# Performance work log

Measured on AMD Instinct MI355X. Metric: run time of the kernel, lower is better.

Reference implementation:

```python
import jax, jax.numpy as jnp
import numpy as np

EPS = 1e-5  # torch BatchNorm1d default eps
NUM_CLASSES = 10


def setup_inputs() -> dict:
    key = jax.random.key(0)
    ks = jax.random.split(key, 8)
    N, M, D = 8192, 8192, 256
    h1, h2 = 128, 64
    x = jax.random.normal(ks[0], (N, D), dtype=jnp.float32)
    x_n = jax.random.normal(ks[1], (M, D), dtype=jnp.float32)
    y_n = jax.random.randint(ks[2], (M,), 0, NUM_CLASSES)
    # Linear weights (torch layout [out, in]) and biases
    W0 = jax.random.normal(ks[3], (h1, D), dtype=jnp.float32) * 0.05
    b0 = jnp.zeros((h1,), dtype=jnp.float32)
    W1 = jax.random.normal(ks[4], (h2, h1), dtype=jnp.float32) * 0.05
    b1 = jnp.zeros((h2,), dtype=jnp.float32)
    # BatchNorm1d affine params (torch init: weight=1, bias=0)
    g0 = jnp.ones((h1,), dtype=jnp.float32)
    bt0 = jnp.zeros((h1,), dtype=jnp.float32)
    g1 = jnp.ones((h2,), dtype=jnp.float32)
    bt1 = jnp.zeros((h2,), dtype=jnp.float32)
    return {"x": x, "x_n": x_n, "y_n": y_n,
            "W0": W0, "b0": b0, "g0": g0, "bt0": bt0,
            "W1": W1, "b1": b1, "g1": g1, "bt1": bt1}


def _bn(h, gamma, beta):
    # BatchNorm1d in training mode: batch mean / biased batch var per feature
    m = jnp.mean(h, axis=0)
    v = jnp.var(h, axis=0)
    return gamma * (h - m) / jnp.sqrt(v + EPS) + beta


def _feats(z, params):
    # fcn stack: BatchNorm(Tanh(Linear(z)))
    for W, b, g, bt in params:
        z = _bn(jnp.tanh(z @ W.T + b), g, bt)
    return z


def reference(x, x_n, y_n, W0, b0, g0, bt0, W1, b1, g1, bt1):
    params = [(W0, b0, g0, bt0), (W1, b1, g1, bt1)]
    q = _feats(x, params)    # [N, 64]
    k = _feats(x_n, params)  # [M, 64]
    # euclidean cdist via the quadratic expansion
    d2 = (jnp.sum(q * q, axis=1)[:, None]
          + jnp.sum(k * k, axis=1)[None, :]
          - 2.0 * (q @ k.T))
    sim = jnp.sqrt(jnp.maximum(d2, 1e-12))  # [N, M]
    sim = jnp.max(sim) - sim                 # larger = nearer
    # x != x_n here, so no self-mask branch (matches torch.equal check)
    p = jax.nn.softmax(sim, axis=1)          # [N, M]
    y1h = jax.nn.one_hot(y_n, NUM_CLASSES, dtype=p.dtype)  # [M, C]
    return jnp.clip(p @ y1h, 0.0, 1.0)       # [N, C]
```

## Files before the change

### kernel.cpp

```cpp
#include <hip/hip_runtime.h>
#include <math.h>

#define EPSBN 1e-5f
#define AADD(p, v) __hip_atomic_fetch_add((p), (v), __ATOMIC_RELAXED, __HIP_MEMORY_SCOPE_AGENT)

typedef unsigned short u16;
typedef short bf16x8 __attribute__((ext_vector_type(8)));
typedef float f32x4 __attribute__((ext_vector_type(4)));
typedef float f32x16 __attribute__((ext_vector_type(16)));

constexpr int NROWS = 8192;
constexpr int NCLS = 10;
constexpr int MPAD = 8832;
constexpr int NT_PAD = 138;
constexpr int GY = 8;
constexpr float SCL  = 2.0813689810056077f;
constexpr float SCL2 = -4.1627379620112154f;

constexpr size_t OFF_W0P = 0;
constexpr size_t OFF_H1H = 32768;
constexpr size_t OFF_H1L = OFF_H1H + 1048576;
constexpr size_t OFF_SUM = OFF_H1L + 1048576;
constexpr size_t OFF_W1P = OFF_SUM + 768;
constexpr size_t OFF_B1E = OFF_W1P + 16384;
constexpr size_t OFF_H2  = OFF_B1E + 128;
constexpr size_t OFF_PIDX = OFF_H2 + 1048576;
constexpr size_t OFF_TCLS = OFF_PIDX + MPAD;
constexpr size_t OFF_QB  = OFF_H1H;
constexpr size_t OFF_KB  = OFF_QB + 262144;
constexpr size_t OFF_QN2 = OFF_KB + 282624;
constexpr size_t OFF_KN2 = OFF_QN2 + NROWS;
constexpr size_t OFF_PART = OFF_H2;

__device__ inline u16 f2bf(float f) {
  unsigned u = __float_as_uint(f);
  unsigned r = (u + 0x7fffu + ((u >> 16) & 1u)) >> 16;
  return (u16)r;
}
__device__ inline float bf2f(u16 h) { return __uint_as_float(((unsigned)h) << 16); }

__device__ inline float tanh_fast(float x) {
  float e = __builtin_amdgcn_exp2f(x * 2.88539008f);
  return 1.f - 2.f * __builtin_amdgcn_rcpf(e + 1.f);
}

__device__ inline void glds16(const u16* g, u16* l) {
  __builtin_amdgcn_global_load_lds(
      (const __attribute__((address_space(1))) unsigned int*)g,
      (__attribute__((address_space(3))) unsigned int*)l, 16, 0, 0);
}

__global__ __launch_bounds__(256) void k_prep(
    const float* __restrict__ w0, const int* __restrict__ yn,
    u16* __restrict__ w0p, int* __restrict__ pidx, int* __restrict__ tcls,
    float* __restrict__ sums)
{
  const int B = blockIdx.x;
  const int tid = threadIdx.x;
  if (B < 128) {
    int idx = B * 256 + tid;
    int t = idx & 255;
    float v = w0[idx];
    u16 hi = f2bf(v);
    u16 lo = f2bf(v - bf2f(hi));
    int j = idx >> 8;
    w0p[(t >> 3) * 1024 + j * 8 + (t & 7)] = hi;
    w0p[32768 + (t >> 3) * 1024 + j * 8 + (t & 7)] = lo;
    return;
  }

  __shared__ int cnt[256][NCLS];
  __shared__ int counts[NCLS];
  __shared__ int pst[NCLS + 1];
  const int lane = tid & 63, wv = tid >> 6;
  #pragma unroll
  for (int c = 0; c < NCLS; ++c) cnt[tid][c] = 0;
  __syncthreads();
  for (int i = tid; i < NROWS; i += 256) cnt[tid][yn[i]]++;
  __syncthreads();
  if (tid < NCLS) {
    int s = 0;
    for (int t = 0; t < 256; ++t) s += cnt[t][tid];
    counts[tid] = s;
  }
  __syncthreads();
  if (tid == 0) {
    int run = 0;
    #pragma unroll
    for (int c = 0; c < NCLS; ++c) {
      pst[c] = run;
      run += ((counts[c] + 63) >> 6) << 6;
    }
    pst[NCLS] = run;
  }
  __syncthreads();

  if (B == 128) {
    sums[tid] = 0.f; sums[tid + 256] = 0.f; sums[tid + 512] = 0.f;
    if (tid == 0) {
      #pragma unroll
      for (int c = 0; c < NCLS; ++c) {
        int nt = (counts[c] + 63) >> 6;
        for (int tt = 0; tt < nt; ++tt) tcls[(pst[c] >> 6) + tt] = c;
      }
      for (int tt = pst[NCLS] >> 6; tt < NT_PAD; ++tt) tcls[tt] = NCLS;
    }
    for (int i = tid; i < MPAD; i += 256) {
      bool pad;
      if (i >= pst[NCLS]) pad = true;
      else {
        int c = 0;
        while (i >= pst[c + 1]) ++c;
        pad = (i >= pst[c] + counts[c]);
      }
      if (pad) pidx[i] = -1;
    }
    return;
  }

  const int c = B - 129;
  __shared__ int wsum[4];
  int x = cnt[tid][c];
  int inc = x;
  #pragma unroll
  for (int d = 1; d < 64; d <<= 1) { int y = __shfl_up(inc, d); if (lane >= d) inc += y; }
  if (lane == 63) wsum[wv] = inc;
  __syncthreads();
  int add = 0;
  for (int w2 = 0; w2 < 4; ++w2) if (w2 < wv) add += wsum[w2];
  int base = pst[c] + (inc - x) + add;
  for (int i = tid; i < NROWS; i += 256) {
    if (yn[i] == c) pidx[base++] = i;
  }
}

__global__ __launch_bounds__(256) void k_layer1(
    const float* __restrict__ x, const float* __restrict__ xn,
    const u16* __restrict__ w0p, const float* __restrict__ b0,
    u16* __restrict__ h1h, u16* __restrict__ h1l, float* __restrict__ sums)
{
  const int tid = threadIdx.x;
  const int w = tid >> 6, l = tid & 63;
  const int l15 = l & 15, l4 = l >> 4;
  const int blk = blockIdx.x;
  const int rowHalf = w & 1, colHalf = w >> 1;
  const int r0 = blk * 32 + 16 * rowHalf;
  const int c0 = 64 * colHalf;
  const int b = (blk < 256) ? 0 : 1;
  const float* src = (blk < 256) ? (x + (size_t)blk * 32 * 256)
                                 : (xn + (size_t)(blk - 256) * 32 * 256);
  const float* xrow = src + (size_t)(16 * rowHalf + l15) * 256;

  f32x4 acc[4];
  #pragma unroll
  for (int ct = 0; ct < 4; ++ct) acc[ct] = (f32x4){0.f, 0.f, 0.f, 0.f};

  #pragma unroll
  for (int ks = 0; ks < 8; ++ks) {
    const float* xp = xrow + ks * 32 + l4 * 8;
    f32x4 a0 = *(const f32x4*)xp;
    f32x4 a1 = *(const f32x4*)(xp + 4);
    bf16x8 ah, al_;
    #pragma unroll
    for (int i = 0; i < 4; ++i) {
      u16 h = f2bf(a0[i]); ah[i] = (short)h; al_[i] = (short)f2bf(a0[i] - bf2f(h));
    }
    #pragma unroll
    for (int i = 0; i < 4; ++i) {
      u16 h = f2bf(a1[i]); ah[4 + i] = (short)h; al_[4 + i] = (short)f2bf(a1[i] - bf2f(h));
    }
    const u16* bbase = w0p + (size_t)(ks * 4 + l4) * 1024;
    #pragma unroll
    for (int ct = 0; ct < 4; ++ct) {
      const int col = c0 + 16 * ct + l15;
      bf16x8 bh = *(const bf16x8*)(bbase + col * 8);
      bf16x8 bl = *(const bf16x8*)(bbase + 32768 + col * 8);
      acc[ct] = __builtin_amdgcn_mfma_f32_16x16x32_bf16(ah, bh, acc[ct], 0, 0, 0);
      acc[ct] = __builtin_amdgcn_mfma_f32_16x16x32_bf16(ah, bl, acc[ct], 0, 0, 0);
      acc[ct] = __builtin_amdgcn_mfma_f32_16x16x32_bf16(al_, bh, acc[ct], 0, 0, 0);
    }
  }

  #pragma unroll
  for (int ct = 0; ct < 4; ++ct) {
    const int col = c0 + 16 * ct + l15;
    const float bj = b0[col];
    float s = 0.f, q = 0.f;
    #pragma unroll
    for (int r = 0; r < 4; ++r) {
      float v = tanh_fast(acc[ct][r] + bj);
      const int row = r0 + 4 * l4 + r;
      u16 hi = f2bf(v);
      h1h[(size_t)row * 128 + col] = hi;
      h1l[(size_t)row * 128 + col] = f2bf(v - bf2f(hi));
      s += v; q += v * v;
    }
    s += __shfl_xor(s, 16); s += __shfl_xor(s, 32);
    q += __shfl_xor(q, 16); q += __shfl_xor(q, 32);
    if (l < 16) {
      AADD(&sums[b * 128 + col], s);
      AADD(&sums[256 + b * 128 + col], q);
    }
  }
}

__global__ __launch_bounds__(128) void k_foldp(
    const float* __restrict__ w1, const float* __restrict__ b1,
    const float* __restrict__ g0, const float* __restrict__ bt0,
    const float* __restrict__ sums, u16* __restrict__ w1p, float* __restrict__ b1e)
{
  const int o = blockIdx.x;
  const int j = threadIdx.x;
  __shared__ float red[2][2];
  const float w = w1[o * 128 + j];
  #pragma unroll
  for (int b = 0; b < 2; ++b) {
    float s = sums[b * 128 + j], q = sums[256 + b * 128 + j];
    float m = s * (1.f / 8192.f);
    float v = q * (1.f / 8192.f) - m * m;
    float sc = g0[j] * rsqrtf(v + EPSBN);
    float sh = bt0[j] - m * sc;
    float wsc = w * sc;
    u16 hi = f2bf(wsc);
    u16 lo = f2bf(wsc - bf2f(hi));
    w1p[((size_t)(b * 2 + 0) * 16 + (j >> 3)) * 512 + o * 8 + (j & 7)] = hi;
    w1p[((size_t)(b * 2 + 1) * 16 + (j >> 3)) * 512 + o * 8 + (j & 7)] = lo;
    float a = w * sh;
    #pragma unroll
    for (int off = 32; off; off >>= 1) a += __shfl_xor(a, off);
    if ((j & 63) == 0) red[j >> 6][b] = a;
  }
  __syncthreads();
  if (j < 2) b1e[j * 64 + o] = b1[o] + red[0][j] + red[1][j];
}

__global__ __launch_bounds__(256) void k_layer2(
    const u16* __restrict__ h1h, const u16* __restrict__ h1l,
    const u16* __restrict__ w1p, const float* __restrict__ b1e,
    float* __restrict__ h2, float* __restrict__ sums)
{
  const int tid = threadIdx.x;
  const int w = tid >> 6, l = tid & 63;
  const int l15 = l & 15, l4 = l >> 4;
  const int blk = blockIdx.x;
  const int rowHalf = w & 1, colHalf = w >> 1;
  const int r0 = blk * 32 + 16 * rowHalf;
  const int c0 = 32 * colHalf;
  const int b = blk >> 8;
  const u16* arow_h = h1h + (size_t)(r0 + l15) * 128;
  const u16* arow_l = h1l + (size_t)(r0 + l15) * 128;

  f32x4 acc[2];
  acc[0] = (f32x4){0.f, 0.f, 0.f, 0.f};
  acc[1] = (f32x4){0.f, 0.f, 0.f, 0.f};

  #pragma unroll
  for (int ks = 0; ks < 4; ++ks) {
    bf16x8 ah = *(const bf16x8*)(arow_h + ks * 32 + l4 * 8);
    bf16x8 al_ = *(const bf16x8*)(arow_l + ks * 32 + l4 * 8);
    const u16* bb = w1p + ((size_t)(b * 2) * 16 + ks * 4 + l4) * 512;
    #pragma unroll
    for (int ct = 0; ct < 2; ++ct) {
      const int col = c0 + 16 * ct + l15;
      bf16x8 bh = *(const bf16x8*)(bb + col * 8);
      bf16x8 bl = *(const bf16x8*)(bb + 8192 + col * 8);
      acc[ct] = __builtin_amdgcn_mfma_f32_16x16x32_bf16(ah, bh, acc[ct], 0, 0, 0);
      acc[ct] = __builtin_amdgcn_mfma_f32_16x16x32_bf16(ah, bl, acc[ct], 0, 0, 0);
      acc[ct] = __builtin_amdgcn_mfma_f32_16x16x32_bf16(al_, bh, acc[ct], 0, 0, 0);
    }
  }

  #pragma unroll
  for (int ct = 0; ct < 2; ++ct) {
    const int col = c0 + 16 * ct + l15;
    const float bj = b1e[b * 64 + col];
    float s = 0.f, q = 0.f;
    #pragma unroll
    for (int r = 0; r < 4; ++r) {
      float v = tanh_fast(acc[ct][r] + bj);
      const int row = r0 + 4 * l4 + r;
      h2[(size_t)row * 64 + col] = v;
      s += v; q += v * v;
    }
    s += __shfl_xor(s, 16); s += __shfl_xor(s, 32);
    q += __shfl_xor(q, 16); q += __shfl_xor(q, 32);
    if (l < 16) {
      AADD(&sums[512 + b * 64 + col], s);
      AADD(&sums[640 + b * 64 + col], q);
    }
  }
}

__global__ __launch_bounds__(256) void k_bn2(
    const float* __restrict__ h2, const float* __restrict__ sums,
    const float* __restrict__ g1, const float* __restrict__ bt1,
    const int* __restrict__ pidx,
    u16* __restrict__ qb, float* __restrict__ qn2,
    u16* __restrict__ kb, float* __restrict__ kn2)
{
  const int tid = threadIdx.x;
  const int r = tid >> 6, o = tid & 63;
  const bool isq = (blockIdx.x < 2048);
  const int b = isq ? 0 : 1;
  float s = sums[512 + b * 64 + o], q = sums[640 + b * 64 + o];
  float m = s * (1.f / 8192.f);
  float v = q * (1.f / 8192.f) - m * m;
  float sc = g1[o] * rsqrtf(v + EPSBN);
  float sh = bt1[o] - m * sc;
  if (isq) {
    const int row = blockIdx.x * 4 + r;
    float vv = sc * h2[(size_t)row * 64 + o] + sh;
    qb[(size_t)row * 64 + o] = f2bf(vv);
    float sq = vv * vv;
    #pragma unroll
    for (int off = 32; off; off >>= 1) sq += __shfl_xor(sq, off);
    if (o == 0) qn2[row] = SCL * sq;
  } else {
    const int row = (blockIdx.x - 2048) * 4 + r;
    const int src = pidx[row];
    float vv = 0.f;
    if (src >= 0) vv = sc * h2[(size_t)(NROWS + src) * 64 + o] + sh;
    kb[(size_t)row * 64 + o] = f2bf(vv);
    float sq = vv * vv;
    #pragma unroll
    for (int off = 32; off; off >>= 1) sq += __shfl_xor(sq, off);
    if (o == 0) kn2[row] = (src >= 0) ? SCL * sq : 1e30f;
  }
}

__global__ __launch_bounds__(256, 4) void k_dist(
    const u16* __restrict__ qb, const float* __restrict__ qn2,
    const u16* __restrict__ kb, const float* __restrict__ kn2,
    const int* __restrict__ tcls, float* __restrict__ part)
{
  __shared__ u16 bs[3][4096];
  __shared__ float cls_lds[2 * (NCLS + 1) * 64];
  const int tid = threadIdx.x;
  const int w = tid >> 6, l = tid & 63;
  const int n0 = blockIdx.x * 64;
  const int g = blockIdx.y;
  const int t0 = (g * NT_PAD) / GY, t1 = ((g + 1) * NT_PAD) / GY;

  for (int i = tid; i < 2 * (NCLS + 1) * 64; i += 256) cls_lds[i] = 0.f;

  const int lh = l >> 5;
  const int rb = w >> 1, ch = w & 1;
  const int arow = n0 + 32 * rb + (l & 31);
  bf16x8 aB[4];
  #pragma unroll
  for (int j = 0; j < 4; ++j)
    aB[j] = *(const bf16x8*)(qb + (size_t)arow * 64 + j * 16 + 8 * lh);
  float qnr[16];
  #pragma unroll
  for (int g4 = 0; g4 < 4; ++g4) {
    f32x4 qv = *(const f32x4*)(qn2 + n0 + 32 * rb + 8 * g4 + 4 * lh);
    qnr[4*g4+0] = qv[0]; qnr[4*g4+1] = qv[1]; qnr[4*g4+2] = qv[2]; qnr[4*g4+3] = qv[3];
  }

  int soff[2];
  #pragma unroll
  for (int q = 0; q < 2; ++q)
    soff[q] = (16 * w + 8 * q + (l >> 3)) * 64 + ((l & 7) ^ (l >> 3)) * 8;

  const int colL = 32 * ch + (l & 31);
  const int c7 = colL & 7;

#define STAGE(TT, PB) do { const u16* gp_ = kb + (size_t)(TT) * 4096; \
    u16* lb_ = &bs[PB][0] + w * 1024; \
    glds16(gp_ + soff[0], lb_); \
    glds16(gp_ + soff[1], lb_ + 512); } while (0)

#define FLUSH(CC) do { \
    _Pragma("unroll") for (int r = 0; r < 16; ++r) { \
      run[r] += __shfl_xor(run[r], 1);  run[r] += __shfl_xor(run[r], 2); \
      run[r] += __shfl_xor(run[r], 4);  run[r] += __shfl_xor(run[r], 8); \
      run[r] += __shfl_xor(run[r], 16); } \
    if ((l & 31) == 0) { \
      float* cl_ = cls_lds + ch * 704 + (CC) * 64 + 32 * rb + 4 * lh; \
      _Pragma("unroll") for (int r = 0; r < 16; ++r) cl_[(r & 3) + 8 * (r >> 2)] += run[r]; } \
    _Pragma("unroll") for (int r = 0; r < 16; ++r) run[r] = 0.f; } while (0)

  STAGE(t0, 0);
  if (t0 + 1 < t1) STAGE(t0 + 1, 1);

  float run[16];
  #pragma unroll
  for (int r = 0; r < 16; ++r) run[r] = 0.f;
  int ccur = tcls[t0];
  int p = 0;

  for (int t = t0; t < t1; ++t) {
    if (t + 1 < t1) { asm volatile("s_waitcnt vmcnt(2)" ::: "memory"); }
    else            { asm volatile("s_waitcnt vmcnt(0)" ::: "memory"); }
    __builtin_amdgcn_s_barrier();
    asm volatile("" ::: "memory");

    if (t + 2 < t1) { int pb2 = p + 2; if (pb2 >= 3) pb2 -= 3; STAGE(t + 2, pb2); }

    const int c = tcls[t];
    if (c != ccur) { FLUSH(ccur); ccur = c; }
    const float kv = kn2[t * 64 + colL];

    f32x16 acc0, acc1;
    #pragma unroll
    for (int r = 0; r < 16; ++r) { acc0[r] = 0.f; acc1[r] = 0.f; }
    const char* pb_ = (const char*)&bs[p][0] + colL * 128;
    {
      bf16x8 b0_ = *(const bf16x8*)(pb_ + (((0 + lh) ^ c7) << 4));
      bf16x8 b1_ = *(const bf16x8*)(pb_ + (((2 + lh) ^ c7) << 4));
      bf16x8 b2_ = *(const bf16x8*)(pb_ + (((4 + lh) ^ c7) << 4));
      bf16x8 b3_ = *(const bf16x8*)(pb_ + (((6 + lh) ^ c7) << 4));
      acc0 = __builtin_amdgcn_mfma_f32_32x32x16_bf16(aB[0], b0_, acc0, 0, 0, 0);
      acc1 = __builtin_amdgcn_mfma_f32_32x32x16_bf16(aB[1], b1_, acc1, 0, 0, 0);
      acc0 = __builtin_amdgcn_mfma_f32_32x32x16_bf16(aB[2], b2_, acc0, 0, 0, 0);
      acc1 = __builtin_amdgcn_mfma_f32_32x32x16_bf16(aB[3], b3_, acc1, 0, 0, 0);
    }
    #pragma unroll
    for (int r = 0; r < 16; ++r) {
      float d2 = fmaf(SCL2, acc0[r] + acc1[r], qnr[r] + kv);
      d2 = fmaxf(d2, 2.0813689e-12f);
      run[r] += __builtin_amdgcn_exp2f(-__builtin_amdgcn_sqrtf(d2));
    }
    p = (p == 2) ? 0 : p + 1;
  }
  FLUSH(ccur);
  __syncthreads();

  for (int i = tid; i < (NCLS + 1) * 64; i += 256) {
    const int c = i >> 6, rr = i & 63;
    part[((size_t)g * (NCLS + 1) + c) * NROWS + n0 + rr] = cls_lds[i] + cls_lds[704 + i];
  }
#undef STAGE
#undef FLUSH
}

__global__ __launch_bounds__(256) void k_final(const float* __restrict__ part,
                                               float* __restrict__ out)
{
  const int n = blockIdx.x * 256 + threadIdx.x;
  float sc[NCLS];
  #pragma unroll
  for (int c = 0; c < NCLS; ++c) sc[c] = 0.f;
  for (int g = 0; g < GY; ++g) {
    #pragma unroll
    for (int c = 0; c < NCLS; ++c)
      sc[c] += part[((size_t)g * (NCLS + 1) + c) * NROWS + n];
  }
  float tot = 0.f;
  #pragma unroll
  for (int c = 0; c < NCLS; ++c) tot += sc[c];
  const float inv = 1.f / tot;
  #pragma unroll
  for (int c = 0; c < NCLS; ++c)
    out[(size_t)n * NCLS + c] = fminf(fmaxf(sc[c] * inv, 0.f), 1.f);
}

extern "C" void kernel_launch(void* const* d_in, const int* in_sizes, int n_in,
                              void* d_out, int out_size, void* d_ws, size_t ws_size,
                              hipStream_t stream) {
  const float* x   = (const float*)d_in[0];
  const float* xn  = (const float*)d_in[1];
  const int*   yn  = (const int*)d_in[2];
  const float* W0  = (const float*)d_in[3];
  const float* b0  = (const float*)d_in[4];
  const float* g0  = (const float*)d_in[5];
  const float* bt0 = (const float*)d_in[6];
  const float* W1  = (const float*)d_in[7];
  const float* b1  = (const float*)d_in[8];
  const float* g1  = (const float*)d_in[9];
  const float* bt1 = (const float*)d_in[10];
  float* out = (float*)d_out;
  float* ws  = (float*)d_ws;

  u16*   w0pp = (u16*)(ws + OFF_W0P);
  u16*   h1hp = (u16*)(ws + OFF_H1H);
  u16*   h1lp = (u16*)(ws + OFF_H1L);
  float* sumsp= ws + OFF_SUM;
  u16*   w1pp = (u16*)(ws + OFF_W1P);
  float* b1ep = ws + OFF_B1E;
  float* h2p  = ws + OFF_H2;
  int*   pidxp= (int*)(ws + OFF_PIDX);
  int*   tclsp= (int*)(ws + OFF_TCLS);
  u16*   qbp  = (u16*)(ws + OFF_QB);
  float* qn2p = ws + OFF_QN2;
  u16*   kbp  = (u16*)(ws + OFF_KB);
  float* kn2p = ws + OFF_KN2;
  float* partp= ws + OFF_PART;

  k_prep<<<139, 256, 0, stream>>>(W0, yn, w0pp, pidxp, tclsp, sumsp);
  k_layer1<<<512, 256, 0, stream>>>(x, xn, w0pp, b0, h1hp, h1lp, sumsp);
  k_foldp<<<64, 128, 0, stream>>>(W1, b1, g0, bt0, sumsp, w1pp, b1ep);
  k_layer2<<<512, 256, 0, stream>>>(h1hp, h1lp, w1pp, b1ep, h2p, sumsp);
  k_bn2<<<2048 + MPAD / 4, 256, 0, stream>>>(h2p, sumsp, g1, bt1, pidxp,
                                             qbp, qn2p, kbp, kn2p);
  k_dist<<<dim3(128, GY), 256, 0, stream>>>(qbp, qn2p, kbp, kn2p, tclsp, partp);
  k_final<<<32, 256, 0, stream>>>(partp, out);
}
```

Baseline: 140.9 us.

## Fuse BN1 weight folding into layer2 kernel and double dist grid Y

Removes the separate k_foldp launch. Each layer2 block now computes the BN1 scale and shift from the sums, builds the split bf16 hi/lo folded W1 in shared memory, and computes the folded bias itself. This saves one launch and a global round trip, but repeats the fold work in all 512 blocks and adds a serial 128-step bias loop in 64 threads. Separately, GY for the distance kernel grid goes from 8 to 16, and the partial buffer moves to its own workspace region so it no longer aliases h2.

```diff
diff --git a/kernel.cpp b/kernel.cpp
--- a/kernel.cpp
+++ b/kernel.cpp
@@ -13,7 +13,7 @@
 constexpr int NCLS = 10;
 constexpr int MPAD = 8832;
 constexpr int NT_PAD = 138;
-constexpr int GY = 8;
+constexpr int GY = 16;
 constexpr float SCL  = 2.0813689810056077f;
 constexpr float SCL2 = -4.1627379620112154f;
 
@@ -21,16 +21,14 @@
 constexpr size_t OFF_H1H = 32768;
 constexpr size_t OFF_H1L = OFF_H1H + 1048576;
 constexpr size_t OFF_SUM = OFF_H1L + 1048576;
-constexpr size_t OFF_W1P = OFF_SUM + 768;
-constexpr size_t OFF_B1E = OFF_W1P + 16384;
-constexpr size_t OFF_H2  = OFF_B1E + 128;
+constexpr size_t OFF_H2  = OFF_SUM + 768;
 constexpr size_t OFF_PIDX = OFF_H2 + 1048576;
 constexpr size_t OFF_TCLS = OFF_PIDX + MPAD;
+constexpr size_t OFF_PART = OFF_TCLS + 144;
 constexpr size_t OFF_QB  = OFF_H1H;
 constexpr size_t OFF_KB  = OFF_QB + 262144;
 constexpr size_t OFF_QN2 = OFF_KB + 282624;
 constexpr size_t OFF_KN2 = OFF_QN2 + NROWS;
-constexpr size_t OFF_PART = OFF_H2;
 
 __device__ inline u16 f2bf(float f) {
   unsigned u = __float_as_uint(f);
@@ -204,41 +202,14 @@
   }
 }
 
-__global__ __launch_bounds__(128) void k_foldp(
-    const float* __restrict__ w1, const float* __restrict__ b1,
-    const float* __restrict__ g0, const float* __restrict__ bt0,
-    const float* __restrict__ sums, u16* __restrict__ w1p, float* __restrict__ b1e)
-{
-  const int o = blockIdx.x;
-  const int j = threadIdx.x;
-  __shared__ float red[2][2];
-  const float w = w1[o * 128 + j];
-  #pragma unroll
-  for (int b = 0; b < 2; ++b) {
-    float s = sums[b * 128 + j], q = sums[256 + b * 128 + j];
-    float m = s * (1.f / 8192.f);
-    float v = q * (1.f / 8192.f) - m * m;
-    float sc = g0[j] * rsqrtf(v + EPSBN);
-    float sh = bt0[j] - m * sc;
-    float wsc = w * sc;
-    u16 hi = f2bf(wsc);
-    u16 lo = f2bf(wsc - bf2f(hi));
-    w1p[((size_t)(b * 2 + 0) * 16 + (j >> 3)) * 512 + o * 8 + (j & 7)] = hi;
-    w1p[((size_t)(b * 2 + 1) * 16 + (j >> 3)) * 512 + o * 8 + (j & 7)] = lo;
-    float a = w * sh;
-    #pragma unroll
-    for (int off = 32; off; off >>= 1) a += __shfl_xor(a, off);
-    if ((j & 63) == 0) red[j >> 6][b] = a;
-  }
-  __syncthreads();
-  if (j < 2) b1e[j * 64 + o] = b1[o] + red[0][j] + red[1][j];
-}
-
 __global__ __launch_bounds__(256) void k_layer2(
     const u16* __restrict__ h1h, const u16* __restrict__ h1l,
-    const u16* __restrict__ w1p, const float* __restrict__ b1e,
+    const float* __restrict__ W1, const float* __restrict__ b1,
+    const float* __restrict__ g0, const float* __restrict__ bt0,
     float* __restrict__ h2, float* __restrict__ sums)
 {
+  __shared__ u16 w1l[16384];
+  __shared__ float sc0s[128], sh0s[128], b1es[64];
   const int tid = threadIdx.x;
   const int w = tid >> 6, l = tid & 63;
   const int l15 = l & 15, l4 = l >> 4;
@@ -247,6 +218,31 @@
   const int r0 = blk * 32 + 16 * rowHalf;
   const int c0 = 32 * colHalf;
   const int b = blk >> 8;
+
+  if (tid < 128) {
+    float s = sums[b * 128 + tid], q = sums[256 + b * 128 + tid];
+    float m = s * (1.f / 8192.f);
+    float v = q * (1.f / 8192.f) - m * m;
+    float sc = g0[tid] * rsqrtf(v + EPSBN);
+    sc0s[tid] = sc;
+    sh0s[tid] = bt0[tid] - m * sc;
+  }
+  __syncthreads();
+  for (int e = tid; e < 8192; e += 256) {
+    const int j = e >> 6, o = e & 63;
+    float wv = W1[o * 128 + j];
+    float wsc = wv * sc0s[j];
+    u16 hi = f2bf(wsc);
+    w1l[(j >> 3) * 512 + o * 8 + (j & 7)] = hi;
+    w1l[8192 + (j >> 3) * 512 + o * 8 + (j & 7)] = f2bf(wsc - bf2f(hi));
+  }
+  if (tid < 64) {
+    float a = 0.f;
+    for (int j = 0; j < 128; ++j) a = fmaf(W1[tid * 128 + j], sh0s[j], a);
+    b1es[tid] = b1[tid] + a;
+  }
+  __syncthreads();
+
   const u16* arow_h = h1h + (size_t)(r0 + l15) * 128;
   const u16* arow_l = h1l + (size_t)(r0 + l15) * 128;
 
@@ -258,7 +254,7 @@
   for (int ks = 0; ks < 4; ++ks) {
     bf16x8 ah = *(const bf16x8*)(arow_h + ks * 32 + l4 * 8);
     bf16x8 al_ = *(const bf16x8*)(arow_l + ks * 32 + l4 * 8);
-    const u16* bb = w1p + ((size_t)(b * 2) * 16 + ks * 4 + l4) * 512;
+    const u16* bb = w1l + (size_t)(ks * 4 + l4) * 512;
     #pragma unroll
     for (int ct = 0; ct < 2; ++ct) {
       const int col = c0 + 16 * ct + l15;
@@ -273,7 +269,7 @@
   #pragma unroll
   for (int ct = 0; ct < 2; ++ct) {
     const int col = c0 + 16 * ct + l15;
-    const float bj = b1e[b * 64 + col];
+    const float bj = b1es[col];
     float s = 0.f, q = 0.f;
     #pragma unroll
     for (int r = 0; r < 4; ++r) {
@@ -476,21 +472,18 @@
   u16*   h1hp = (u16*)(ws + OFF_H1H);
   u16*   h1lp = (u16*)(ws + OFF_H1L);
   float* sumsp= ws + OFF_SUM;
-  u16*   w1pp = (u16*)(ws + OFF_W1P);
-  float* b1ep = ws + OFF_B1E;
   float* h2p  = ws + OFF_H2;
   int*   pidxp= (int*)(ws + OFF_PIDX);
   int*   tclsp= (int*)(ws + OFF_TCLS);
+  float* partp= ws + OFF_PART;
   u16*   qbp  = (u16*)(ws + OFF_QB);
   float* qn2p = ws + OFF_QN2;
   u16*   kbp  = (u16*)(ws + OFF_KB);
   float* kn2p = ws + OFF_KN2;
-  float* partp= ws + OFF_PART;
 
   k_prep<<<139, 256, 0, stream>>>(W0, yn, w0pp, pidxp, tclsp, sumsp);
   k_layer1<<<512, 256, 0, stream>>>(x, xn, w0pp, b0, h1hp, h1lp, sumsp);
-  k_foldp<<<64, 128, 0, stream>>>(W1, b1, g0, bt0, sumsp, w1pp, b1ep);
-  k_layer2<<<512, 256, 0, stream>>>(h1hp, h1lp, w1pp, b1ep, h2p, sumsp);
+  k_layer2<<<512, 256, 0, stream>>>(h1hp, h1lp, W1, b1, g0, bt0, h2p, sumsp);
   k_bn2<<<2048 + MPAD / 4, 256, 0, stream>>>(h2p, sumsp, g1, bt1, pidxp,
                                              qbp, qn2p, kbp, kn2p);
   k_dist<<<dim3(128, GY), 256, 0, stream>>>(qbp, qn2p, kbp, kn2p, tclsp, partp);
```

After: 168.2 us. +19.4%, slower.
